# Performance work log

Hardware: AMD Instinct MI355X
Metric: run time of the kernel (lower is better)

Reference implementation:

```python
import jax, jax.numpy as jnp
import numpy as np

B, S, E, H = 8, 2048, 256, 8
LN_EPS = 1e-5


def setup_inputs() -> dict:
    key = jax.random.key(0)
    ks = jax.random.split(key, 5)
    x = jax.random.normal(ks[0], (B, S, E), dtype=jnp.float32)
    Wq = jax.random.normal(ks[1], (E, E), dtype=jnp.float32) * 0.02
    Wk = jax.random.normal(ks[2], (E, E), dtype=jnp.float32) * 0.02
    Wv = jax.random.normal(ks[3], (E, E), dtype=jnp.float32) * 0.02
    bias_table = jax.random.normal(ks[4], (2 * S - 1, H), dtype=jnp.float32) * 0.02
    ln_gamma = jnp.ones((E,), dtype=jnp.float32)
    ln_beta = jnp.zeros((E,), dtype=jnp.float32)
    return {"x": x, "Wq": Wq, "Wk": Wk, "Wv": Wv,
            "bias_table": bias_table, "ln_gamma": ln_gamma, "ln_beta": ln_beta}


def reference(x, Wq, Wk, Wv, bias_table, ln_gamma, ln_beta):
    b, s, e = x.shape
    h = bias_table.shape[1]
    d = e // h
    scale = e ** (-0.5)  # note: original scales by emb_size**-0.5, not head_dim

    # torch nn.Linear(bias=False): y = x @ W.T
    q = (x @ Wq.T).reshape(b, s, h, d).transpose(0, 2, 1, 3)  # [b,h,s,d]
    k = (x @ Wk.T).reshape(b, s, h, d).transpose(0, 2, 1, 3)
    v = (x @ Wv.T).reshape(b, s, h, d).transpose(0, 2, 1, 3)

    # full attention matrix (the chunked torch loop computes exactly this)
    attn = jax.nn.softmax(jnp.einsum('bhqd,bhkd->bhqk', q, k) * scale, axis=-1)

    # relative bias: index[i,j] = i - j + (s-1); added AFTER softmax (faithful)
    idx = jnp.arange(s)[:, None] - jnp.arange(s)[None, :] + (s - 1)  # [s,s]
    rel_bias = bias_table[idx].transpose(2, 0, 1)  # [h,s,s]
    attn = attn + rel_bias[None]

    out = jnp.einsum('bhqk,bhkd->bhqd', attn, v)
    out = out.transpose(0, 2, 1, 3).reshape(b, s, e)

    # LayerNorm over last dim
    mu = jnp.mean(out, axis=-1, keepdims=True)
    var = jnp.var(out, axis=-1, keepdims=True)
    out = (out - mu) * jax.lax.rsqrt(var + LN_EPS) * ln_gamma + ln_beta
    return out
```

## Files before the change

### kernel.cpp

```cpp
#include <hip/hip_runtime.h>
#include <math.h>

typedef unsigned short u16;
typedef unsigned int u32;
typedef __attribute__((ext_vector_type(8))) short short8;
typedef __attribute__((ext_vector_type(16))) float floatx16;

constexpr int CB = 8;
constexpr int CS = 2048;
constexpr int CE = 256;
constexpr int CH = 8;
constexpr int CD = 32;
constexpr float CLN_EPS = 1e-5f;
constexpr float QSC = 0.0625f * 1.44269504088896341f;

constexpr int QP = 40;
constexpr int VP = 72;
constexpr int XP = 264;
constexpr int RST = 4104;

__device__ inline u32 fbits(float f) { union { float f; u32 u; } c; c.f = f; return c.u; }
__device__ inline u32 pack2(float a, float b) {
  return __builtin_amdgcn_perm(fbits(b) + 0x8000u, fbits(a) + 0x8000u, 0x07060302u);
}
__device__ inline u16 bf1(float a) { return (u16)((fbits(a) + 0x8000u) >> 16); }
__device__ inline short8 ld8(const u16* p) {
  union { uint4 q; short8 v; } c; c.q = *(const uint4*)p; return c.v;
}

#if __has_builtin(__builtin_amdgcn_permlane32_swap)
__device__ inline void swap32(u32& a, u32& b) {
  typedef __attribute__((ext_vector_type(2))) unsigned int uint2v;
  uint2v r = __builtin_amdgcn_permlane32_swap(a, b, false, false);
  a = r[0]; b = r[1];
}
#else
__device__ inline void swap32(u32& a, u32& b) {
  int hi = (threadIdx.x >> 5) & 1;
  u32 sa = (u32)__shfl_xor((int)a, 32);
  u32 sb = (u32)__shfl_xor((int)b, 32);
  u32 na = hi ? sb : a;
  u32 nb = hi ? b : sa;
  a = na; b = nb;
}
#endif

__global__ __launch_bounds__(256) void cvt_w_kernel(const float* __restrict__ Wq,
                                                    const float* __restrict__ Wk,
                                                    const float* __restrict__ Wv,
                                                    u16* __restrict__ Wb) {
  int gid = blockIdx.x * 256 + threadIdx.x;
  int which = gid >> 14;
  int off = (gid & 16383) * 4;
  const float* W = (which == 0) ? Wq : (which == 1) ? Wk : Wv;
  float4 f = *(const float4*)&W[off];
  uint2 o; o.x = pack2(f.x, f.y); o.y = pack2(f.z, f.w);
  *(uint2*)&Wb[(size_t)which * CE * CE + off] = o;
}

__global__ __launch_bounds__(256) void rev_prep_kernel(const float* __restrict__ table,
                                                       u16* __restrict__ revg) {
  int gid = blockIdx.x * 256 + threadIdx.x;
  if (gid >= 64 * 513) return;
  int g = gid / 513;
  int j0 = (gid - g * 513) * 8;
  int h = g >> 3, p = g & 7;
  u16 vals[8];
#pragma unroll
  for (int t = 0; t < 8; ++t) {
    int src = 4094 - (j0 + t + p);
    vals[t] = (src >= 0) ? bf1(table[(size_t)src * CH + h]) : (u16)0;
  }
  *(uint4*)&revg[(size_t)g * RST + j0] = *(uint4*)vals;
}

__global__ __launch_bounds__(256, 3) void qkv_mfma_kernel(
    const float* __restrict__ x, const u16* __restrict__ Wb,
    u16* __restrict__ qb, u16* __restrict__ kb, u16* __restrict__ vb) {
  __shared__ __attribute__((aligned(16))) u16 Xs[32 * XP];
  const int m0 = blockIdx.x * 32;
  const int nh = blockIdx.y;
  const int tid = threadIdx.x;
  const int lane = tid & 63, wv = tid >> 6;
  const int lm = lane & 31, lg = lane >> 5;

#pragma unroll
  for (int it = 0; it < 8; ++it) {
    int c = tid + 256 * it;
    int row = c >> 6, f4 = c & 63;
    float4 f = *(const float4*)&x[(size_t)(m0 + row) * CE + f4 * 4];
    uint2 o; o.x = pack2(f.x, f.y); o.y = pack2(f.z, f.w);
    *(uint2*)&Xs[row * XP + f4 * 4] = o;
  }
  __syncthreads();

  short8 xf[16];
#pragma unroll
  for (int kt = 0; kt < 16; ++kt) xf[kt] = ld8(&Xs[lm * XP + kt * 16 + lg * 8]);

  const int sg = m0 + lm;
  const int bI = sg >> 11, sI = sg & (CS - 1);

  for (int j = 0; j < 3; ++j) {
    int t = nh * 12 + wv * 3 + j;
    int which = t >> 3;
    int nc = (t & 7) * 32;
    int h = nc >> 5;
    const u16* Wsrc = Wb + (size_t)which * CE * CE;
    floatx16 acc;
#pragma unroll
    for (int i = 0; i < 16; ++i) acc[i] = 0.f;
    {
      short8 wf[8];
#pragma unroll
      for (int kt = 0; kt < 8; ++kt)
        wf[kt] = ld8(&Wsrc[(size_t)(nc + lm) * CE + kt * 16 + lg * 8]);
#pragma unroll
      for (int kt = 0; kt < 8; ++kt)
        acc = __builtin_amdgcn_mfma_f32_32x32x16_bf16(wf[kt], xf[kt], acc, 0, 0, 0);
    }
    {
      short8 wf[8];
#pragma unroll
      for (int kt = 0; kt < 8; ++kt)
        wf[kt] = ld8(&Wsrc[(size_t)(nc + lm) * CE + (kt + 8) * 16 + lg * 8]);
#pragma unroll
      for (int kt = 0; kt < 8; ++kt)
        acc = __builtin_amdgcn_mfma_f32_32x32x16_bf16(wf[kt], xf[kt + 8], acc, 0, 0, 0);
    }
    if (which < 2) {
      u16* dst = which ? kb : qb;
      float scl = which ? 1.0f : QSC;
      u32 D[8];
#pragma unroll
      for (int g = 0; g < 8; ++g)
        D[g] = pack2(acc[2 * g] * scl, acc[2 * g + 1] * scl);
      swap32(D[0], D[2]); swap32(D[1], D[3]);
      swap32(D[4], D[6]); swap32(D[5], D[7]);
      size_t base = (((size_t)bI * CH + h) * CS + sI) * CD;
      uint4 U0; U0.x = D[0]; U0.y = D[1]; U0.z = D[2]; U0.w = D[3];
      uint4 U1; U1.x = D[4]; U1.y = D[5]; U1.z = D[6]; U1.w = D[7];
      *(uint4*)&dst[base + 8 * lg] = U0;
      *(uint4*)&dst[base + 16 + 8 * lg] = U1;
    } else {
#pragma unroll
      for (int r = 0; r < 16; ++r) {
        int d = (r & 3) + 8 * (r >> 2) + 4 * lg;
        vb[(((size_t)bI * CH + h) * CD + d) * CS + sI] = bf1(acc[r]);
      }
    }
  }
}

__global__ __launch_bounds__(256, 4) void attn_mfma_kernel(
    const u16* __restrict__ qm, const u16* __restrict__ km,
    const u16* __restrict__ vm, const u16* __restrict__ revg,
    float* __restrict__ out) {
  __shared__ __attribute__((aligned(16))) u16 Ks[2][64 * QP];
  __shared__ __attribute__((aligned(16))) u16 Vt[2][32 * VP];

  const int q0 = blockIdx.x * 128;
  const int bh = blockIdx.y;
  const int b = bh >> 3, h = bh & 7;
  const int tid = threadIdx.x;
  const int lane = tid & 63, wv = tid >> 6;
  const int lm = lane & 31, lg = lane >> 5;
  const u16* qbp = qm + (size_t)bh * CS * CD;
  const u16* kbp = km + (size_t)bh * CS * CD;
  const u16* vbp = vm + (size_t)bh * CD * CS;

  const int qrow = wv * 32 + lm;
  const u16* qp = qbp + (size_t)(q0 + qrow) * CD;
  short8 qa0 = ld8(qp + lg * 8);
  short8 qa1 = ld8(qp + 16 + lg * 8);

  const int Xb = 2047 - q0 - qrow + lg * 8;
  const int pp = Xb & 7;
  const u16* bp = revg + (size_t)(h * 8 + pp) * RST + (Xb - pp);

  const int krow = tid >> 2, kch = tid & 3;
  const int vrow = tid >> 3, vch = tid & 7;
  uint4 kreg = *(const uint4*)&kbp[(size_t)krow * CD + kch * 8];
  uint4 vreg = *(const uint4*)&vbp[(size_t)vrow * CS + vch * 8];

  floatx16 acc_e, acc_b;
#pragma unroll
  for (int i = 0; i < 16; ++i) { acc_e[i] = 0.f; acc_b[i] = 0.f; }
  float l = 0.f;

  for (int k0 = 0; k0 < CS; k0 += 64) {
    const int p = (k0 >> 6) & 1;
    *(uint4*)&Ks[p][krow * QP + kch * 8] = kreg;
    *(uint4*)&Vt[p][vrow * VP + vch * 8] = vreg;
    if (k0 + 64 < CS) {
      kreg = *(const uint4*)&kbp[(size_t)(k0 + 64 + krow) * CD + kch * 8];
      vreg = *(const uint4*)&vbp[(size_t)vrow * CS + (k0 + 64) + vch * 8];
    }
    uint4 bu0 = *(const uint4*)&bp[k0];
    uint4 bu1 = *(const uint4*)&bp[k0 + 16];
    uint4 bu2 = *(const uint4*)&bp[k0 + 32];
    uint4 bu3 = *(const uint4*)&bp[k0 + 48];
    __syncthreads();

    floatx16 sc0, sc1;
#pragma unroll
    for (int i = 0; i < 16; ++i) { sc0[i] = 0.f; sc1[i] = 0.f; }
    {
      short8 a00 = ld8(&Ks[p][lm * QP + lg * 8]);
      short8 a01 = ld8(&Ks[p][lm * QP + 16 + lg * 8]);
      short8 a10 = ld8(&Ks[p][(32 + lm) * QP + lg * 8]);
      short8 a11 = ld8(&Ks[p][(32 + lm) * QP + 16 + lg * 8]);
      sc0 = __builtin_amdgcn_mfma_f32_32x32x16_bf16(a00, qa0, sc0, 0, 0, 0);
      sc0 = __builtin_amdgcn_mfma_f32_32x32x16_bf16(a01, qa1, sc0, 0, 0, 0);
      sc1 = __builtin_amdgcn_mfma_f32_32x32x16_bf16(a10, qa0, sc1, 0, 0, 0);
      sc1 = __builtin_amdgcn_mfma_f32_32x32x16_bf16(a11, qa1, sc1, 0, 0, 0);
    }

#pragma unroll
    for (int ct = 0; ct < 2; ++ct) {
      floatx16& sc = ct ? sc1 : sc0;
      u32 P[8];
#pragma unroll
      for (int g = 0; g < 8; ++g) {
        float e0 = __builtin_amdgcn_exp2f(sc[2 * g]);
        float e1 = __builtin_amdgcn_exp2f(sc[2 * g + 1]);
        l += e0 + e1;
        P[g] = pack2(e0, e1);
      }
      swap32(P[0], P[2]); swap32(P[1], P[3]);
      swap32(P[4], P[6]); swap32(P[5], P[7]);
      union { u32 u[4]; short8 v; } B0, B1;
      B0.u[0] = P[0]; B0.u[1] = P[1]; B0.u[2] = P[2]; B0.u[3] = P[3];
      B1.u[0] = P[4]; B1.u[1] = P[5]; B1.u[2] = P[6]; B1.u[3] = P[7];
      short8 va0 = ld8(&Vt[p][lm * VP + ct * 32 + lg * 8]);
      short8 va1 = ld8(&Vt[p][lm * VP + ct * 32 + 16 + lg * 8]);
      acc_e = __builtin_amdgcn_mfma_f32_32x32x16_bf16(va0, B0.v, acc_e, 0, 0, 0);
      acc_e = __builtin_amdgcn_mfma_f32_32x32x16_bf16(va1, B1.v, acc_e, 0, 0, 0);
      union { uint4 q; short8 v; } Bb0, Bb1;
      Bb0.q = ct ? bu2 : bu0;
      Bb1.q = ct ? bu3 : bu1;
      acc_b = __builtin_amdgcn_mfma_f32_32x32x16_bf16(va0, Bb0.v, acc_b, 0, 0, 0);
      acc_b = __builtin_amdgcn_mfma_f32_32x32x16_bf16(va1, Bb1.v, acc_b, 0, 0, 0);
    }
  }

  l += __shfl_xor(l, 32);
  float rl = __builtin_amdgcn_rcpf(l);
  size_t ob = ((size_t)b * CS + q0 + qrow) * CE + h * CD;
#pragma unroll
  for (int g = 0; g < 4; ++g) {
    float4 r4;
    r4.x = acc_e[4 * g + 0] * rl + acc_b[4 * g + 0];
    r4.y = acc_e[4 * g + 1] * rl + acc_b[4 * g + 1];
    r4.z = acc_e[4 * g + 2] * rl + acc_b[4 * g + 2];
    r4.w = acc_e[4 * g + 3] * rl + acc_b[4 * g + 3];
    *(float4*)&out[ob + 8 * g + 4 * lg] = r4;
  }
}

__global__ __launch_bounds__(256) void ln_kernel(float* __restrict__ io,
                                                 const float* __restrict__ gamma,
                                                 const float* __restrict__ beta) {
  int tid = threadIdx.x;
  size_t row = (size_t)blockIdx.x * 4 + (tid >> 6);
  int c = (tid & 63) * 4;
  float4 v = *(const float4*)&io[row * CE + c];
  float s1 = v.x + v.y + v.z + v.w;
  float s2 = v.x * v.x + v.y * v.y + v.z * v.z + v.w * v.w;
#pragma unroll
  for (int off = 1; off < 64; off <<= 1) {
    s1 += __shfl_xor(s1, off);
    s2 += __shfl_xor(s2, off);
  }
  float mu = s1 * (1.0f / CE);
  float var = s2 * (1.0f / CE) - mu * mu;
  float rs = rsqrtf(var + CLN_EPS);
  float4 g = *(const float4*)&gamma[c];
  float4 be = *(const float4*)&beta[c];
  float4 o;
  o.x = (v.x - mu) * rs * g.x + be.x;
  o.y = (v.y - mu) * rs * g.y + be.y;
  o.z = (v.z - mu) * rs * g.z + be.z;
  o.w = (v.w - mu) * rs * g.w + be.w;
  *(float4*)&io[row * CE + c] = o;
}

extern "C" void kernel_launch(void* const* d_in, const int* in_sizes, int n_in,
                              void* d_out, int out_size, void* d_ws, size_t ws_size,
                              hipStream_t stream) {
  (void)in_sizes; (void)n_in; (void)out_size; (void)ws_size;
  const float* x          = (const float*)d_in[0];
  const float* Wq         = (const float*)d_in[1];
  const float* Wk         = (const float*)d_in[2];
  const float* Wv         = (const float*)d_in[3];
  const float* bias_table = (const float*)d_in[4];
  const float* gamma      = (const float*)d_in[5];
  const float* beta       = (const float*)d_in[6];
  float* out = (float*)d_out;

  u16* ws = (u16*)d_ws;
  u16* Wb = ws;
  u16* qb = Wb + 3 * CE * CE;
  u16* kb = qb + (size_t)CB * CH * CS * CD;
  u16* vb = kb + (size_t)CB * CH * CS * CD;
  u16* revg = vb + (size_t)CB * CH * CS * CD;

  cvt_w_kernel<<<dim3(192), dim3(256), 0, stream>>>(Wq, Wk, Wv, Wb);
  rev_prep_kernel<<<dim3(129), dim3(256), 0, stream>>>(bias_table, revg);
  qkv_mfma_kernel<<<dim3(512, 2), dim3(256), 0, stream>>>(x, Wb, qb, kb, vb);
  attn_mfma_kernel<<<dim3(CS / 128, CB * CH), dim3(256), 0, stream>>>(qb, kb, vb, revg, out);
  ln_kernel<<<dim3(CB * CS / 4), dim3(256), 0, stream>>>(out, gamma, beta);
}
```

Measured before the change: 182.3 us.

## Enlarge attention key tile, compute softmax sum via MFMA, merge prep kernels

The attention kernel now stages 128 keys per iteration instead of 64, which halves the number of barriers and loop trips. Bias loads move inside the per-32-key inner loop. The softmax denominator is accumulated by an extra MFMA that multiplies the probability tiles by a ones matrix, replacing the scalar adds and the cross-lane shuffle. Separately, the two prep kernels are merged into one launch, and the QKV kernel loads X fragments per half to reduce register pressure. In exchange the attention kernel uses more LDS and one more accumulator, which may lower occupancy, and sums the probabilities in bf16-rounded form.

```diff
diff --git a/kernel.cpp b/kernel.cpp
--- a/kernel.cpp
+++ b/kernel.cpp
@@ -15,7 +15,7 @@
 constexpr float QSC = 0.0625f * 1.44269504088896341f;
 
 constexpr int QP = 40;
-constexpr int VP = 72;
+constexpr int VP2 = 136;
 constexpr int XP = 264;
 constexpr int RST = 4104;
 
@@ -45,33 +45,32 @@
 }
 #endif
 
-__global__ __launch_bounds__(256) void cvt_w_kernel(const float* __restrict__ Wq,
-                                                    const float* __restrict__ Wk,
-                                                    const float* __restrict__ Wv,
-                                                    u16* __restrict__ Wb) {
+__global__ __launch_bounds__(256) void prep_kernel(
+    const float* __restrict__ Wq, const float* __restrict__ Wk,
+    const float* __restrict__ Wv, const float* __restrict__ table,
+    u16* __restrict__ Wb, u16* __restrict__ revg) {
   int gid = blockIdx.x * 256 + threadIdx.x;
-  int which = gid >> 14;
-  int off = (gid & 16383) * 4;
-  const float* W = (which == 0) ? Wq : (which == 1) ? Wk : Wv;
-  float4 f = *(const float4*)&W[off];
-  uint2 o; o.x = pack2(f.x, f.y); o.y = pack2(f.z, f.w);
-  *(uint2*)&Wb[(size_t)which * CE * CE + off] = o;
-}
-
-__global__ __launch_bounds__(256) void rev_prep_kernel(const float* __restrict__ table,
-                                                       u16* __restrict__ revg) {
-  int gid = blockIdx.x * 256 + threadIdx.x;
-  if (gid >= 64 * 513) return;
-  int g = gid / 513;
-  int j0 = (gid - g * 513) * 8;
-  int h = g >> 3, p = g & 7;
-  u16 vals[8];
-#pragma unroll
-  for (int t = 0; t < 8; ++t) {
-    int src = 4094 - (j0 + t + p);
-    vals[t] = (src >= 0) ? bf1(table[(size_t)src * CH + h]) : (u16)0;
-  }
-  *(uint4*)&revg[(size_t)g * RST + j0] = *(uint4*)vals;
+  if (gid < 49152) {
+    int which = gid >> 14;
+    int off = (gid & 16383) * 4;
+    const float* W = (which == 0) ? Wq : (which == 1) ? Wk : Wv;
+    float4 f = *(const float4*)&W[off];
+    uint2 o; o.x = pack2(f.x, f.y); o.y = pack2(f.z, f.w);
+    *(uint2*)&Wb[(size_t)which * CE * CE + off] = o;
+  } else {
+    int gid2 = gid - 49152;
+    if (gid2 >= 64 * 513) return;
+    int g = gid2 / 513;
+    int j0 = (gid2 - g * 513) * 8;
+    int h = g >> 3, p = g & 7;
+    u16 vals[8];
+#pragma unroll
+    for (int t = 0; t < 8; ++t) {
+      int src = 4094 - (j0 + t + p);
+      vals[t] = (src >= 0) ? bf1(table[(size_t)src * CH + h]) : (u16)0;
+    }
+    *(uint4*)&revg[(size_t)g * RST + j0] = *(uint4*)vals;
+  }
 }
 
 __global__ __launch_bounds__(256, 3) void qkv_mfma_kernel(
@@ -94,10 +93,6 @@
   }
   __syncthreads();
 
-  short8 xf[16];
-#pragma unroll
-  for (int kt = 0; kt < 16; ++kt) xf[kt] = ld8(&Xs[lm * XP + kt * 16 + lg * 8]);
-
   const int sg = m0 + lm;
   const int bI = sg >> 11, sI = sg & (CS - 1);
 
@@ -110,23 +105,17 @@
     floatx16 acc;
 #pragma unroll
     for (int i = 0; i < 16; ++i) acc[i] = 0.f;
-    {
-      short8 wf[8];
-#pragma unroll
-      for (int kt = 0; kt < 8; ++kt)
-        wf[kt] = ld8(&Wsrc[(size_t)(nc + lm) * CE + kt * 16 + lg * 8]);
+#pragma unroll
+    for (int half = 0; half < 2; ++half) {
+      short8 wf[8], xf[8];
+#pragma unroll
+      for (int kt = 0; kt < 8; ++kt) {
+        wf[kt] = ld8(&Wsrc[(size_t)(nc + lm) * CE + (half * 8 + kt) * 16 + lg * 8]);
+        xf[kt] = ld8(&Xs[lm * XP + (half * 8 + kt) * 16 + lg * 8]);
+      }
 #pragma unroll
       for (int kt = 0; kt < 8; ++kt)
         acc = __builtin_amdgcn_mfma_f32_32x32x16_bf16(wf[kt], xf[kt], acc, 0, 0, 0);
-    }
-    {
-      short8 wf[8];
-#pragma unroll
-      for (int kt = 0; kt < 8; ++kt)
-        wf[kt] = ld8(&Wsrc[(size_t)(nc + lm) * CE + (kt + 8) * 16 + lg * 8]);
-#pragma unroll
-      for (int kt = 0; kt < 8; ++kt)
-        acc = __builtin_amdgcn_mfma_f32_32x32x16_bf16(wf[kt], xf[kt + 8], acc, 0, 0, 0);
     }
     if (which < 2) {
       u16* dst = which ? kb : qb;
@@ -156,8 +145,8 @@
     const u16* __restrict__ qm, const u16* __restrict__ km,
     const u16* __restrict__ vm, const u16* __restrict__ revg,
     float* __restrict__ out) {
-  __shared__ __attribute__((aligned(16))) u16 Ks[2][64 * QP];
-  __shared__ __attribute__((aligned(16))) u16 Vt[2][32 * VP];
+  __shared__ __attribute__((aligned(16))) u16 Ks[2][128 * QP];
+  __shared__ __attribute__((aligned(16))) u16 Vt[2][32 * VP2];
 
   const int q0 = blockIdx.x * 128;
   const int bh = blockIdx.y;
@@ -178,53 +167,51 @@
   const int pp = Xb & 7;
   const u16* bp = revg + (size_t)(h * 8 + pp) * RST + (Xb - pp);
 
-  const int krow = tid >> 2, kch = tid & 3;
-  const int vrow = tid >> 3, vch = tid & 7;
-  uint4 kreg = *(const uint4*)&kbp[(size_t)krow * CD + kch * 8];
-  uint4 vreg = *(const uint4*)&vbp[(size_t)vrow * CS + vch * 8];
-
-  floatx16 acc_e, acc_b;
-#pragma unroll
-  for (int i = 0; i < 16; ++i) { acc_e[i] = 0.f; acc_b[i] = 0.f; }
-  float l = 0.f;
-
-  for (int k0 = 0; k0 < CS; k0 += 64) {
-    const int p = (k0 >> 6) & 1;
-    *(uint4*)&Ks[p][krow * QP + kch * 8] = kreg;
-    *(uint4*)&Vt[p][vrow * VP + vch * 8] = vreg;
-    if (k0 + 64 < CS) {
-      kreg = *(const uint4*)&kbp[(size_t)(k0 + 64 + krow) * CD + kch * 8];
-      vreg = *(const uint4*)&vbp[(size_t)vrow * CS + (k0 + 64) + vch * 8];
-    }
-    uint4 bu0 = *(const uint4*)&bp[k0];
-    uint4 bu1 = *(const uint4*)&bp[k0 + 16];
-    uint4 bu2 = *(const uint4*)&bp[k0 + 32];
-    uint4 bu3 = *(const uint4*)&bp[k0 + 48];
+  short8 ones;
+#pragma unroll
+  for (int i = 0; i < 8; ++i) ones[i] = (short)0x3F80;
+
+  const int krow = tid >> 1, kc = (tid & 1) * 16;
+  const int vrow = tid >> 3, vc = (tid & 7) * 16;
+  uint4 kr0 = *(const uint4*)&kbp[(size_t)krow * CD + kc];
+  uint4 kr1 = *(const uint4*)&kbp[(size_t)krow * CD + kc + 8];
+  uint4 vr0 = *(const uint4*)&vbp[(size_t)vrow * CS + vc];
+  uint4 vr1 = *(const uint4*)&vbp[(size_t)vrow * CS + vc + 8];
+
+  floatx16 acc_e, acc_b, acc_l;
+#pragma unroll
+  for (int i = 0; i < 16; ++i) { acc_e[i] = 0.f; acc_b[i] = 0.f; acc_l[i] = 0.f; }
+
+  for (int k0 = 0; k0 < CS; k0 += 128) {
+    const int p = (k0 >> 7) & 1;
+    *(uint4*)&Ks[p][krow * QP + kc] = kr0;
+    *(uint4*)&Ks[p][krow * QP + kc + 8] = kr1;
+    *(uint4*)&Vt[p][vrow * VP2 + vc] = vr0;
+    *(uint4*)&Vt[p][vrow * VP2 + vc + 8] = vr1;
+    if (k0 + 128 < CS) {
+      kr0 = *(const uint4*)&kbp[(size_t)(k0 + 128 + krow) * CD + kc];
+      kr1 = *(const uint4*)&kbp[(size_t)(k0 + 128 + krow) * CD + kc + 8];
+      vr0 = *(const uint4*)&vbp[(size_t)vrow * CS + (k0 + 128) + vc];
+      vr1 = *(const uint4*)&vbp[(size_t)vrow * CS + (k0 + 128) + vc + 8];
+    }
     __syncthreads();
 
-    floatx16 sc0, sc1;
-#pragma unroll
-    for (int i = 0; i < 16; ++i) { sc0[i] = 0.f; sc1[i] = 0.f; }
-    {
-      short8 a00 = ld8(&Ks[p][lm * QP + lg * 8]);
-      short8 a01 = ld8(&Ks[p][lm * QP + 16 + lg * 8]);
-      short8 a10 = ld8(&Ks[p][(32 + lm) * QP + lg * 8]);
-      short8 a11 = ld8(&Ks[p][(32 + lm) * QP + 16 + lg * 8]);
-      sc0 = __builtin_amdgcn_mfma_f32_32x32x16_bf16(a00, qa0, sc0, 0, 0, 0);
-      sc0 = __builtin_amdgcn_mfma_f32_32x32x16_bf16(a01, qa1, sc0, 0, 0, 0);
-      sc1 = __builtin_amdgcn_mfma_f32_32x32x16_bf16(a10, qa0, sc1, 0, 0, 0);
-      sc1 = __builtin_amdgcn_mfma_f32_32x32x16_bf16(a11, qa1, sc1, 0, 0, 0);
-    }
-
-#pragma unroll
-    for (int ct = 0; ct < 2; ++ct) {
-      floatx16& sc = ct ? sc1 : sc0;
+#pragma unroll
+    for (int ct = 0; ct < 4; ++ct) {
+      uint4 bua = *(const uint4*)&bp[k0 + ct * 32];
+      uint4 bub = *(const uint4*)&bp[k0 + ct * 32 + 16];
+      short8 a00 = ld8(&Ks[p][(ct * 32 + lm) * QP + lg * 8]);
+      short8 a01 = ld8(&Ks[p][(ct * 32 + lm) * QP + 16 + lg * 8]);
+      floatx16 sc;
+#pragma unroll
+      for (int i = 0; i < 16; ++i) sc[i] = 0.f;
+      sc = __builtin_amdgcn_mfma_f32_32x32x16_bf16(a00, qa0, sc, 0, 0, 0);
+      sc = __builtin_amdgcn_mfma_f32_32x32x16_bf16(a01, qa1, sc, 0, 0, 0);
       u32 P[8];
 #pragma unroll
       for (int g = 0; g < 8; ++g) {
         float e0 = __builtin_amdgcn_exp2f(sc[2 * g]);
         float e1 = __builtin_amdgcn_exp2f(sc[2 * g + 1]);
-        l += e0 + e1;
         P[g] = pack2(e0, e1);
       }
       swap32(P[0], P[2]); swap32(P[1], P[3]);
@@ -232,20 +219,20 @@
       union { u32 u[4]; short8 v; } B0, B1;
       B0.u[0] = P[0]; B0.u[1] = P[1]; B0.u[2] = P[2]; B0.u[3] = P[3];
       B1.u[0] = P[4]; B1.u[1] = P[5]; B1.u[2] = P[6]; B1.u[3] = P[7];
-      short8 va0 = ld8(&Vt[p][lm * VP + ct * 32 + lg * 8]);
-      short8 va1 = ld8(&Vt[p][lm * VP + ct * 32 + 16 + lg * 8]);
+      short8 va0 = ld8(&Vt[p][lm * VP2 + ct * 32 + lg * 8]);
+      short8 va1 = ld8(&Vt[p][lm * VP2 + ct * 32 + 16 + lg * 8]);
       acc_e = __builtin_amdgcn_mfma_f32_32x32x16_bf16(va0, B0.v, acc_e, 0, 0, 0);
       acc_e = __builtin_amdgcn_mfma_f32_32x32x16_bf16(va1, B1.v, acc_e, 0, 0, 0);
+      acc_l = __builtin_amdgcn_mfma_f32_32x32x16_bf16(ones, B0.v, acc_l, 0, 0, 0);
+      acc_l = __builtin_amdgcn_mfma_f32_32x32x16_bf16(ones, B1.v, acc_l, 0, 0, 0);
       union { uint4 q; short8 v; } Bb0, Bb1;
-      Bb0.q = ct ? bu2 : bu0;
-      Bb1.q = ct ? bu3 : bu1;
+      Bb0.q = bua; Bb1.q = bub;
       acc_b = __builtin_amdgcn_mfma_f32_32x32x16_bf16(va0, Bb0.v, acc_b, 0, 0, 0);
       acc_b = __builtin_amdgcn_mfma_f32_32x32x16_bf16(va1, Bb1.v, acc_b, 0, 0, 0);
     }
   }
 
-  l += __shfl_xor(l, 32);
-  float rl = __builtin_amdgcn_rcpf(l);
+  float rl = __builtin_amdgcn_rcpf(acc_l[0]);
   size_t ob = ((size_t)b * CS + q0 + qrow) * CE + h * CD;
 #pragma unroll
   for (int g = 0; g < 4; ++g) {
@@ -305,8 +292,7 @@
   u16* vb = kb + (size_t)CB * CH * CS * CD;
   u16* revg = vb + (size_t)CB * CH * CS * CD;
 
-  cvt_w_kernel<<<dim3(192), dim3(256), 0, stream>>>(Wq, Wk, Wv, Wb);
-  rev_prep_kernel<<<dim3(129), dim3(256), 0, stream>>>(bias_table, revg);
+  prep_kernel<<<dim3(321), dim3(256), 0, stream>>>(Wq, Wk, Wv, bias_table, Wb, revg);
   qkv_mfma_kernel<<<dim3(512, 2), dim3(256), 0, stream>>>(x, Wb, qb, kb, vb);
   attn_mfma_kernel<<<dim3(CS / 128, CB * CH), dim3(256), 0, stream>>>(qb, kb, vb, revg, out);
   ln_kernel<<<dim3(CB * CS / 4), dim3(256), 0, stream>>>(out, gamma, beta);
```

Result: slower. 190.8 us (+4.7%).
